# Kernel tuning notes

Hardware: AMD Instinct MI355X
Metric: run time of the kernel (lower is better)

The kernel has to match this reference:

```python
import jax, jax.numpy as jnp
import numpy as np

# Config matching init_kwargs / input_specs
B, H, S, D = 4, 16, 4096, 64
BLK = 16          # sparsity_block
W = 32            # num_local_blocks (banded causal layout: block i attends blocks i-W+1..i)


def setup_inputs() -> dict:
    key = jax.random.key(0)
    kq, kk, kv = jax.random.split(key, 3)
    query = jax.random.normal(kq, (B, H, S, D), dtype=jnp.float16)
    k = jax.random.normal(kk, (B, H, S, D), dtype=jnp.float16)
    value = jax.random.normal(kv, (B, H, S, D), dtype=jnp.float16)
    return {"query": query, "key": k, "value": value}


def reference(query, key, value):
    b, h, s, d = query.shape
    nb = s // BLK
    scale = 1.0 / np.sqrt(d)

    qb = query.reshape(b, h, nb, BLK, d)
    kb = key.reshape(b, h, nb, BLK, d)
    vb = value.reshape(b, h, nb, BLK, d)

    # Banded causal block layout: for query block i, kv block indices i-W+1 .. i
    i = jnp.arange(nb)[:, None]                    # [nb,1]
    w = jnp.arange(W)[None, :]                     # [1,W]
    kv_idx = i - (W - 1) + w                       # [nb,W]
    valid = kv_idx >= 0
    idxc = jnp.clip(kv_idx, 0, nb - 1)

    kg = kb[:, :, idxc]                            # [B,H,nb,W,BLK,D] gathered K blocks
    vg = vb[:, :, idxc]                            # [B,H,nb,W,BLK,D]

    # SDD: block-sparse QK^T, only active blocks are computed
    scores = jnp.einsum('bhnqd,bhnwkd->bhnqwk', qb, kg).astype(jnp.float32) * scale

    # causal + validity mask on global token positions
    q_pos = (jnp.arange(nb) * BLK)[:, None, None, None] + jnp.arange(BLK)[None, :, None, None]  # [nb,BLK,1,1]
    k_pos = (kv_idx * BLK)[:, None, :, None] + jnp.arange(BLK)[None, None, None, :]             # [nb,1,W,BLK]
    mask = (k_pos <= q_pos) & valid[:, None, :, None]
    scores = jnp.where(mask, scores, -jnp.inf)

    # sparse softmax over all active key positions of each query row
    p = jax.nn.softmax(scores.reshape(b, h, nb, BLK, W * BLK), axis=-1)
    p = p.reshape(b, h, nb, BLK, W, BLK).astype(jnp.float16)

    # DSD: sparse-probabilities x dense-V
    out = jnp.einsum('bhnqwk,bhnwkd->bhnqd', p, vg)
    return out.reshape(b, h, s, d)
```

## Files before the change

kernel.cpp:

```cpp
#include <hip/hip_runtime.h>

#define SS 4096
#define DD 64
#define WW 32
#define NEG (-1e30f)
#define CSCALE 0.1803368801f
#define DEFER_THR 8.0f

typedef _Float16 half8_t __attribute__((ext_vector_type(8)));
typedef __fp16 fp16x2_t __attribute__((ext_vector_type(2)));
typedef float float4_t __attribute__((ext_vector_type(4)));

static __device__ __forceinline__ unsigned pk(float a, float b) {
  fp16x2_t h = __builtin_amdgcn_cvt_pkrtz(a, b);
  return __builtin_bit_cast(unsigned, h);
}

static __device__ __forceinline__ half8_t cvt8(const float* p) {
  float4_t a = *(const float4_t*)p;
  float4_t b = *(const float4_t*)(p + 4);
  union { half8_t h; unsigned u[4]; } x;
  x.u[0] = pk(a[0], a[1]);
  x.u[1] = pk(a[2], a[3]);
  x.u[2] = pk(b[0], b[1]);
  x.u[3] = pk(b[2], b[3]);
  return x.h;
}

static __device__ __forceinline__ half8_t lds_frag16(const unsigned short* p) {
  union { half8_t h; uint4 u; } x;
  x.u = *(const uint4*)p;
  return x.h;
}

static __device__ __forceinline__ int ksig(int r) {
  return ((r & 3) ^ ((r >> 3) & 3)) | ((r & 2) << 1);
}

__global__ __launch_bounds__(512, 6)
void sparse_attn_kernel(const float* __restrict__ Q,
                        const float* __restrict__ K,
                        const float* __restrict__ V,
                        float* __restrict__ O) {
  __shared__ __align__(16) unsigned short kl[2][64 * 64];
  __shared__ __align__(16) unsigned short vl[2][2][64 * 32];

  const int lin = blockIdx.x;
  const int xcd = lin & 7;
  const int logical = (lin >> 3) + xcd * ((int)gridDim.x >> 3);
  const int bh = logical >> 5;
  const int i0 = (logical & 31) * 8;

  const int tid = threadIdx.x;
  const int wave = tid >> 6;
  const int lane = tid & 63;
  const int t = lane & 15;
  const int q = lane >> 4;

  const size_t base = (size_t)bh * SS * DD;
  const float* Qb = Q + base;
  const float* Kb = K + base;
  const float* Vb = V + base;

  const int i = i0 + wave;

  const float* qrow = Qb + (size_t)(i * 16 + t) * DD;
  const half8_t qf0 = cvt8(qrow + q * 8);
  const half8_t qf1 = cvt8(qrow + 32 + q * 8);

  const int prow0 = ((t >> 2) << 3) + (t & 3);
  int koff[2][2];
#pragma unroll
  for (int p = 0; p < 2; ++p)
#pragma unroll
    for (int ro = 0; ro < 2; ++ro) {
      const int rowb = p * 32 + prow0 + ro * 4;
      koff[p][ro] = rowb * 64 + ((q ^ ksig(rowb)) << 3);
    }
  const int vslot8 = (q ^ ((t >> 1) & 3)) << 3;

  float4_t accO[4];
#pragma unroll
  for (int c = 0; c < 4; ++c) accO[c] = {0.f, 0.f, 0.f, 0.f};
  float m_run = NEG;
  float l_run = 0.0f;

  const int lo_blk = (i0 - (WW - 1)) > 0 ? (i0 - (WW - 1)) : 0;
  const int Ulo = lo_blk >> 2;
  const int Uhi = (i0 + 7) >> 2;
  const int nit = Uhi - Ulo + 1;

  const int kr_ = tid >> 3;
  const int kc8 = tid & 7;
  const int kstoff = kr_ * 64 + ((kc8 ^ ksig(kr_)) << 3);

  const int vpair = tid >> 8;
  const int vdl = tid & 31;
  const int vn0 = ((tid >> 5) & 7) * 4;
  const int vstoff = (vdl * 2) * 32 + (vn0 ^ ((vdl & 3) << 3));

  const float* kg = Kb + (size_t)(Ulo * 64 + kr_) * DD + kc8 * 8;
  const float* vg = Vb + (size_t)(Ulo * 64 + vpair * 32 + vn0) * DD + vdl * 2;

  float4_t kv[2];
  float2 vv[4];

  auto load_raw = [&]() {
    kv[0] = *(const float4_t*)kg;
    kv[1] = *(const float4_t*)(kg + 4);
#pragma unroll
    for (int rr = 0; rr < 4; ++rr) vv[rr] = *(const float2*)(vg + rr * DD);
    kg += 64 * DD;
    vg += 64 * DD;
  };

  auto store_stage = [&](int bf) {
    uint4 w;
    w.x = pk(kv[0][0], kv[0][1]);
    w.y = pk(kv[0][2], kv[0][3]);
    w.z = pk(kv[1][0], kv[1][1]);
    w.w = pk(kv[1][2], kv[1][3]);
    *(uint4*)&kl[bf][kstoff] = w;
    uint2 wlo, whi;
    wlo.x = pk(vv[0].x, vv[1].x);
    wlo.y = pk(vv[2].x, vv[3].x);
    whi.x = pk(vv[0].y, vv[1].y);
    whi.y = pk(vv[2].y, vv[3].y);
    unsigned short* vd = &vl[bf][vpair][vstoff];
    *(uint2*)vd = wlo;
    *(uint2*)(vd + 32) = whi;
  };

  load_raw();

  for (int it = 0; it < nit; ++it) {
    const int U = Ulo + it;
    const int bf = it & 1;
    store_stage(bf);
    __syncthreads();
    if (it + 1 < nit) load_raw();

    if (4 * U <= i && 4 * U >= i - 34) {
      float4_t st[4];
#pragma unroll
      for (int g = 0; g < 4; ++g) st[g] = {0.f, 0.f, 0.f, 0.f};
#pragma unroll
      for (int p = 0; p < 2; ++p)
#pragma unroll
        for (int ro = 0; ro < 2; ++ro) {
          half8_t kf0 = lds_frag16(&kl[bf][koff[p][ro]]);
          half8_t kf1 = lds_frag16(&kl[bf][koff[p][ro] ^ 32]);
          st[p * 2 + ro] =
              __builtin_amdgcn_mfma_f32_16x16x32_f16(kf0, qf0, st[p * 2 + ro], 0, 0, 0);
          st[p * 2 + ro] =
              __builtin_amdgcn_mfma_f32_16x16x32_f16(kf1, qf1, st[p * 2 + ro], 0, 0, 0);
        }

      float s[4][4];
      if ((4 * U < i - (WW - 1)) || (4 * U + 3 >= i)) {
#pragma unroll
        for (int p = 0; p < 2; ++p) {
          const int jj = 4 * U + 2 * p + (q >> 1);
          const bool bad = (jj < i - (WW - 1)) || (jj > i);
          const bool dg = (jj == i);
          const int kr = (q & 1) << 3;
#pragma unroll
          for (int ro = 0; ro < 2; ++ro)
#pragma unroll
            for (int r = 0; r < 4; ++r) {
              float v = st[p * 2 + ro][r] * CSCALE;
              if (bad || (dg && (kr + ro * 4 + r > t))) v = NEG;
              s[p * 2 + ro][r] = v;
            }
        }
      } else {
#pragma unroll
        for (int g = 0; g < 4; ++g)
#pragma unroll
          for (int r = 0; r < 4; ++r) s[g][r] = st[g][r] * CSCALE;
      }

      float vmax = NEG;
#pragma unroll
      for (int g = 0; g < 4; ++g)
#pragma unroll
        for (int r = 0; r < 4; ++r) vmax = fmaxf(vmax, s[g][r]);
      vmax = fmaxf(vmax, __shfl_xor(vmax, 16));
      vmax = fmaxf(vmax, __shfl_xor(vmax, 32));

      if (__any(vmax > m_run + DEFER_THR)) {
        const float m_new = fmaxf(m_run, vmax);
        const float alpha = __builtin_exp2f(m_run - m_new);
        l_run *= alpha;
#pragma unroll
        for (int c = 0; c < 4; ++c)
#pragma unroll
          for (int r = 0; r < 4; ++r) accO[c][r] *= alpha;
        m_run = m_new;
      }

      float rs = 0.f;
#pragma unroll
      for (int g = 0; g < 4; ++g)
#pragma unroll
        for (int r = 0; r < 4; ++r) {
          s[g][r] = __builtin_exp2f(s[g][r] - m_run);
          rs += s[g][r];
        }
      rs += __shfl_xor(rs, 16);
      rs += __shfl_xor(rs, 32);
      l_run += rs;

      union { half8_t h; unsigned u[4]; } pb0, pb1;
      pb0.u[0] = pk(s[0][0], s[0][1]);
      pb0.u[1] = pk(s[0][2], s[0][3]);
      pb0.u[2] = pk(s[1][0], s[1][1]);
      pb0.u[3] = pk(s[1][2], s[1][3]);
      pb1.u[0] = pk(s[2][0], s[2][1]);
      pb1.u[1] = pk(s[2][2], s[2][3]);
      pb1.u[2] = pk(s[3][0], s[3][1]);
      pb1.u[3] = pk(s[3][2], s[3][3]);

      const unsigned short* v0 = vl[bf][0];
      const unsigned short* v1 = vl[bf][1];
#pragma unroll
      for (int c = 0; c < 4; ++c) {
        const int voff = (c * 16 + t) * 32 + vslot8;
        half8_t va0 = lds_frag16(&v0[voff]);
        half8_t va1 = lds_frag16(&v1[voff]);
        accO[c] = __builtin_amdgcn_mfma_f32_16x16x32_f16(va0, pb0.h, accO[c], 0, 0, 0);
        accO[c] = __builtin_amdgcn_mfma_f32_16x16x32_f16(va1, pb1.h, accO[c], 0, 0, 0);
      }
    }
  }

  const float inv_l = 1.0f / l_run;
  float* orow = O + base + (size_t)(i * 16 + t) * DD;
#pragma unroll
  for (int c = 0; c < 4; ++c) {
    float4_t ov;
#pragma unroll
    for (int r = 0; r < 4; ++r) ov[r] = accO[c][r] * inv_l;
    *(float4_t*)(orow + c * 16 + q * 4) = ov;
  }
}

extern "C" void kernel_launch(void* const* d_in, const int* in_sizes, int n_in,
                              void* d_out, int out_size, void* d_ws, size_t ws_size,
                              hipStream_t stream) {
  const float* Q = (const float*)d_in[0];
  const float* K = (const float*)d_in[1];
  const float* V = (const float*)d_in[2];
  float* O = (float*)d_out;
  sparse_attn_kernel<<<dim3(2048), dim3(512), 0, stream>>>(Q, K, V, O);
}
```

Measured before the change: 297.6 us.

## Split work into 4-wave blocks with a wider swizzled K/V LDS layout

Halves the query blocks per workgroup, from 8 waves to 4, and doubles the grid. Each thread now loads twice as much K/V per stage, and V is stored in a single 64-wide XOR-swizzled LDS tile. The goal is finer-grained scheduling and better latency hiding. The cost is roughly double redundant K/V loading and conversion per query block, plus a 48KB dynamic LDS request that may cap occupancy.

```diff
diff --git a/kernel.cpp b/kernel.cpp
--- a/kernel.cpp
+++ b/kernel.cpp
@@ -37,19 +37,20 @@
   return ((r & 3) ^ ((r >> 3) & 3)) | ((r & 2) << 1);
 }
 
-__global__ __launch_bounds__(512, 6)
+__global__ __launch_bounds__(256, 3)
 void sparse_attn_kernel(const float* __restrict__ Q,
                         const float* __restrict__ K,
                         const float* __restrict__ V,
                         float* __restrict__ O) {
-  __shared__ __align__(16) unsigned short kl[2][64 * 64];
-  __shared__ __align__(16) unsigned short vl[2][2][64 * 32];
+  extern __shared__ __align__(16) unsigned short smem[];
+  unsigned short* kl = smem;
+  unsigned short* vq = smem + 2 * 4096;
 
   const int lin = blockIdx.x;
   const int xcd = lin & 7;
   const int logical = (lin >> 3) + xcd * ((int)gridDim.x >> 3);
-  const int bh = logical >> 5;
-  const int i0 = (logical & 31) * 8;
+  const int bh = logical >> 6;
+  const int i0 = (logical & 63) * 4;
 
   const int tid = threadIdx.x;
   const int wave = tid >> 6;
@@ -77,7 +78,7 @@
       const int rowb = p * 32 + prow0 + ro * 4;
       koff[p][ro] = rowb * 64 + ((q ^ ksig(rowb)) << 3);
     }
-  const int vslot8 = (q ^ ((t >> 1) & 3)) << 3;
+  const int voff0 = t * 64 + (((q ^ (t >> 1)) & 7) << 3);
 
   float4_t accO[4];
 #pragma unroll
@@ -87,48 +88,58 @@
 
   const int lo_blk = (i0 - (WW - 1)) > 0 ? (i0 - (WW - 1)) : 0;
   const int Ulo = lo_blk >> 2;
-  const int Uhi = (i0 + 7) >> 2;
+  const int Uhi = (i0 + 3) >> 2;
   const int nit = Uhi - Ulo + 1;
 
-  const int kr_ = tid >> 3;
-  const int kc8 = tid & 7;
-  const int kstoff = kr_ * 64 + ((kc8 ^ ksig(kr_)) << 3);
-
-  const int vpair = tid >> 8;
+  const int kr_ = tid >> 2;
+  const int kcg = tid & 3;
+  const int kst0 = kr_ * 64 + ((((kcg * 2) ^ ksig(kr_)) & 7) << 3);
+  const int kst1 = kr_ * 64 + ((((kcg * 2 + 1) ^ ksig(kr_)) & 7) << 3);
+
   const int vdl = tid & 31;
-  const int vn0 = ((tid >> 5) & 7) * 4;
-  const int vstoff = (vdl * 2) * 32 + (vn0 ^ ((vdl & 3) << 3));
-
-  const float* kg = Kb + (size_t)(Ulo * 64 + kr_) * DD + kc8 * 8;
-  const float* vg = Vb + (size_t)(Ulo * 64 + vpair * 32 + vn0) * DD + vdl * 2;
-
-  float4_t kv[2];
-  float2 vv[4];
+  const int vg8 = (tid >> 5) & 7;
+  const int vst0 = (2 * vdl) * 64 + (((vg8 ^ vdl) & 7) << 3);
+
+  const float* kg = Kb + (size_t)(Ulo * 64 + kr_) * DD + kcg * 16;
+  const float* vg = Vb + (size_t)(Ulo * 64 + vg8 * 8) * DD + vdl * 2;
+
+  float4_t kv[4];
+  float2 vv[8];
 
   auto load_raw = [&]() {
-    kv[0] = *(const float4_t*)kg;
-    kv[1] = *(const float4_t*)(kg + 4);
-#pragma unroll
-    for (int rr = 0; rr < 4; ++rr) vv[rr] = *(const float2*)(vg + rr * DD);
+#pragma unroll
+    for (int ii = 0; ii < 4; ++ii) kv[ii] = *(const float4_t*)(kg + ii * 4);
+#pragma unroll
+    for (int rr = 0; rr < 8; ++rr) vv[rr] = *(const float2*)(vg + rr * DD);
     kg += 64 * DD;
     vg += 64 * DD;
   };
 
   auto store_stage = [&](int bf) {
-    uint4 w;
-    w.x = pk(kv[0][0], kv[0][1]);
-    w.y = pk(kv[0][2], kv[0][3]);
-    w.z = pk(kv[1][0], kv[1][1]);
-    w.w = pk(kv[1][2], kv[1][3]);
-    *(uint4*)&kl[bf][kstoff] = w;
-    uint2 wlo, whi;
+    uint4 w0, w1;
+    w0.x = pk(kv[0][0], kv[0][1]);
+    w0.y = pk(kv[0][2], kv[0][3]);
+    w0.z = pk(kv[1][0], kv[1][1]);
+    w0.w = pk(kv[1][2], kv[1][3]);
+    w1.x = pk(kv[2][0], kv[2][1]);
+    w1.y = pk(kv[2][2], kv[2][3]);
+    w1.z = pk(kv[3][0], kv[3][1]);
+    w1.w = pk(kv[3][2], kv[3][3]);
+    unsigned short* kd = kl + bf * 4096;
+    *(uint4*)(kd + kst0) = w0;
+    *(uint4*)(kd + kst1) = w1;
+    uint4 wlo, whi;
     wlo.x = pk(vv[0].x, vv[1].x);
     wlo.y = pk(vv[2].x, vv[3].x);
+    wlo.z = pk(vv[4].x, vv[5].x);
+    wlo.w = pk(vv[6].x, vv[7].x);
     whi.x = pk(vv[0].y, vv[1].y);
     whi.y = pk(vv[2].y, vv[3].y);
-    unsigned short* vd = &vl[bf][vpair][vstoff];
-    *(uint2*)vd = wlo;
-    *(uint2*)(vd + 32) = whi;
+    whi.z = pk(vv[4].y, vv[5].y);
+    whi.w = pk(vv[6].y, vv[7].y);
+    unsigned short* vd = vq + bf * 4096 + vst0;
+    *(uint4*)vd = wlo;
+    *(uint4*)(vd + 64) = whi;
   };
 
   load_raw();
@@ -141,6 +152,7 @@
     if (it + 1 < nit) load_raw();
 
     if (4 * U <= i && 4 * U >= i - 34) {
+      const unsigned short* kd = kl + bf * 4096;
       float4_t st[4];
 #pragma unroll
       for (int g = 0; g < 4; ++g) st[g] = {0.f, 0.f, 0.f, 0.f};
@@ -148,8 +160,8 @@
       for (int p = 0; p < 2; ++p)
 #pragma unroll
         for (int ro = 0; ro < 2; ++ro) {
-          half8_t kf0 = lds_frag16(&kl[bf][koff[p][ro]]);
-          half8_t kf1 = lds_frag16(&kl[bf][koff[p][ro] ^ 32]);
+          half8_t kf0 = lds_frag16(&kd[koff[p][ro]]);
+          half8_t kf1 = lds_frag16(&kd[koff[p][ro] ^ 32]);
           st[p * 2 + ro] =
               __builtin_amdgcn_mfma_f32_16x16x32_f16(kf0, qf0, st[p * 2 + ro], 0, 0, 0);
           st[p * 2 + ro] =
@@ -221,13 +233,12 @@
       pb1.u[2] = pk(s[3][0], s[3][1]);
       pb1.u[3] = pk(s[3][2], s[3][3]);
 
-      const unsigned short* v0 = vl[bf][0];
-      const unsigned short* v1 = vl[bf][1];
+      const unsigned short* vd = vq + bf * 4096;
 #pragma unroll
       for (int c = 0; c < 4; ++c) {
-        const int voff = (c * 16 + t) * 32 + vslot8;
-        half8_t va0 = lds_frag16(&v0[voff]);
-        half8_t va1 = lds_frag16(&v1[voff]);
+        const int vo = c * 1024 + voff0;
+        half8_t va0 = lds_frag16(&vd[vo]);
+        half8_t va1 = lds_frag16(&vd[vo ^ 32]);
         accO[c] = __builtin_amdgcn_mfma_f32_16x16x32_f16(va0, pb0.h, accO[c], 0, 0, 0);
         accO[c] = __builtin_amdgcn_mfma_f32_16x16x32_f16(va1, pb1.h, accO[c], 0, 0, 0);
       }
@@ -252,5 +263,5 @@
   const float* K = (const float*)d_in[1];
   const float* V = (const float*)d_in[2];
   float* O = (float*)d_out;
-  sparse_attn_kernel<<<dim3(2048), dim3(512), 0, stream>>>(Q, K, V, O);
-}
+  sparse_attn_kernel<<<dim3(4096), dim3(256), 49152, stream>>>(Q, K, V, O);
+}
```

Measured after the change: 262.4 us. 1.13x faster.
